# Optimization experiments

Measured on AMD Instinct MI355X. Metric: run time of the kernel, lower is better.

## Reference

```python
import math
import jax, jax.numpy as jnp
import numpy as np
from jax.scipy.special import gammaln, xlogy

HEADS = 8
DIM_KEY = 64
DIM_VALUE = 64
NUM_REL_POS_FEATURES = 192
DIM = 768
SEQ = 2048
BATCH = 2


def get_positional_embed(seq_len: int, feature_size: int) -> jnp.ndarray:
    # distances: [2n-1]
    distances = jnp.arange(-seq_len + 1, seq_len, dtype=jnp.float32)
    f = feature_size // 6  # 3 basis classes, then doubled with sign term
    absd = jnp.abs(distances)[:, None]  # [2n-1, 1]
    # exponential basis
    max_range = math.log(seq_len) / math.log(2.0)
    half_life = 2.0 ** jnp.linspace(3.0, max_range, f)[None, :]
    exp_feat = jnp.exp(-math.log(2.0) / half_life * absd)
    # central mask basis
    center_widths = 2.0 ** jnp.arange(1, f + 1, dtype=jnp.float32) - 1.0
    cmask = (center_widths[None, :] > absd).astype(jnp.float32)
    # gamma pdf basis
    stddev = seq_len / (2.0 * f)
    start_mean = seq_len / f
    mean = jnp.linspace(start_mean, float(seq_len), f)[None, :]
    concentration = (mean / stddev) ** 2
    rate = mean / stddev ** 2
    log_unnorm = xlogy(concentration - 1.0, absd) - rate * absd
    log_norm = gammaln(concentration) - concentration * jnp.log(rate)
    probs = jnp.exp(log_unnorm - log_norm) + 1e-8
    gamma_feat = probs / jnp.max(probs, axis=-1, keepdims=True)
    emb = jnp.concatenate([exp_feat, cmask, gamma_feat], axis=-1)  # [2n-1, 3f]
    return jnp.concatenate([emb, jnp.sign(distances)[:, None] * emb], axis=-1)  # [2n-1, 6f]


def relative_shift(x: jnp.ndarray) -> jnp.ndarray:
    # x: [b, h, n, 2n-1] -> [b, h, n, n] via Transformer-XL shift trick
    x = jnp.concatenate([jnp.zeros_like(x[..., :1]), x], axis=-1)
    b, h, t1, t2 = x.shape  # t2 = 2n
    x = x.reshape(b, h, t2, t1)[:, :, 1:, :].reshape(b, h, t1, t2 - 1)
    return x[..., : (t2 + 1) // 2]


def setup_inputs() -> dict:
    key = jax.random.key(0)
    ks = jax.random.split(key, 9)
    d_inner = HEADS * DIM_KEY
    d_vinner = HEADS * DIM_VALUE
    sc = 1.0 / math.sqrt(DIM)
    return {
        "x": jax.random.normal(ks[0], (BATCH, SEQ, DIM), dtype=jnp.float32),
        "Wq": jax.random.normal(ks[1], (DIM, d_inner), dtype=jnp.float32) * sc,
        "Wk": jax.random.normal(ks[2], (DIM, d_inner), dtype=jnp.float32) * sc,
        "Wv": jax.random.normal(ks[3], (DIM, d_vinner), dtype=jnp.float32) * sc,
        "Wrel": jax.random.normal(ks[4], (NUM_REL_POS_FEATURES, d_inner), dtype=jnp.float32) * (1.0 / math.sqrt(NUM_REL_POS_FEATURES)),
        "rel_content_bias": jax.random.normal(ks[5], (1, HEADS, 1, DIM_KEY), dtype=jnp.float32),
        "rel_pos_bias": jax.random.normal(ks[6], (1, HEADS, 1, DIM_KEY), dtype=jnp.float32),
        "Wo": jax.random.normal(ks[7], (d_vinner, DIM), dtype=jnp.float32) * (1.0 / math.sqrt(d_vinner)),
        "bo": jax.random.normal(ks[8], (DIM,), dtype=jnp.float32) * 0.01,
    }


def reference(x, Wq, Wk, Wv, Wrel, rel_content_bias, rel_pos_bias, Wo, bo):
    b, n, _ = x.shape
    scale = DIM_KEY ** -0.5
    # projections -> [b, h, n, d]
    q = (x @ Wq).reshape(b, n, HEADS, DIM_KEY).transpose(0, 2, 1, 3) * scale
    k = (x @ Wk).reshape(b, n, HEADS, DIM_KEY).transpose(0, 2, 1, 3)
    v = (x @ Wv).reshape(b, n, HEADS, DIM_VALUE).transpose(0, 2, 1, 3)
    content_logits = jnp.einsum("bhid,bhjd->bhij", q + rel_content_bias, k)
    positions = get_positional_embed(n, NUM_REL_POS_FEATURES)  # [2n-1, F]
    rel_k = (positions @ Wrel).reshape(2 * n - 1, HEADS, DIM_KEY).transpose(1, 0, 2)  # [h, 2n-1, d]
    rel_logits = jnp.einsum("bhid,hjd->bhij", q + rel_pos_bias, rel_k)
    rel_logits = relative_shift(rel_logits)  # [b, h, n, n]
    attn = jax.nn.softmax(content_logits + rel_logits, axis=-1)
    out = jnp.einsum("bhij,bhjd->bhid", attn, v)  # [b, h, n, dv]
    out = out.transpose(0, 2, 1, 3).reshape(b, n, HEADS * DIM_VALUE)
    return out @ Wo + bo
```

## Files before the change

kernel.cpp:

```cpp
#include <hip/hip_runtime.h>
#include <hip/hip_bf16.h>
#include <math.h>


typedef _Float16 f16x8 __attribute__((ext_vector_type(8)));
typedef _Float16 f16x4 __attribute__((ext_vector_type(4)));
typedef float f32x4 __attribute__((ext_vector_type(4)));

#define MFMA16(a, b, c) __builtin_amdgcn_mfma_f32_16x16x32_f16((a), (b), (c), 0, 0, 0)

#define GL16(gp, lp)                                                       \
  __builtin_amdgcn_global_load_lds(                                        \
      (const __attribute__((address_space(1))) void*)(gp),                 \
      (__attribute__((address_space(3))) void*)(lp), 16, 0, 0)

__device__ __forceinline__ float dpp_fmax16(float x) {
  int v;
  v = __builtin_amdgcn_update_dpp(0, __float_as_int(x), 0xB1, 0xf, 0xf, true);
  x = fmaxf(x, __int_as_float(v));
  v = __builtin_amdgcn_update_dpp(0, __float_as_int(x), 0x4E, 0xf, 0xf, true);
  x = fmaxf(x, __int_as_float(v));
  v = __builtin_amdgcn_update_dpp(0, __float_as_int(x), 0x141, 0xf, 0xf, true);
  x = fmaxf(x, __int_as_float(v));
  v = __builtin_amdgcn_update_dpp(0, __float_as_int(x), 0x140, 0xf, 0xf, true);
  x = fmaxf(x, __int_as_float(v));
  return x;
}

__global__ __launch_bounds__(256) void prep_kernel(
    const float* __restrict__ x, const float* __restrict__ Wq,
    const float* __restrict__ Wk, const float* __restrict__ Wv,
    const float* __restrict__ Wrel, const float* __restrict__ Wo,
    _Float16* __restrict__ xb, _Float16* __restrict__ wqkvt,
    _Float16* __restrict__ wrelt, _Float16* __restrict__ wot,
    _Float16* __restrict__ posb) {
  __shared__ float tile[32][33];
  const int t = threadIdx.x;
  int bid = blockIdx.x;
  if (bid < 3072) {
    const int idx = bid * 256 + t;
    float4 v = ((const float4*)x)[idx];
    f16x4 o;
    o[0] = (_Float16)v.x; o[1] = (_Float16)v.y; o[2] = (_Float16)v.z; o[3] = (_Float16)v.w;
    ((f16x4*)xb)[idx] = o;
    return;
  }
  bid -= 3072;
  if (bid < 1632) {
    const float* in; _Float16* out; int K_, N_, bx, by;
    if (bid < 1152) {
      const int z = bid / 384, rem = bid % 384;
      in = (z == 0) ? Wq : (z == 1) ? Wk : Wv;
      out = wqkvt + (size_t)z * 512 * 768;
      K_ = 768; N_ = 512; bx = rem & 15; by = rem >> 4;
    } else if (bid < 1248) {
      const int rem = bid - 1152;
      in = Wrel; out = wrelt;
      K_ = 192; N_ = 512; bx = rem & 15; by = rem >> 4;
    } else {
      const int rem = bid - 1248;
      in = Wo; out = wot;
      K_ = 512; N_ = 768; bx = rem % 24; by = rem / 24;
    }
    const int k0 = by * 32, n0 = bx * 32;
    const int tr = t >> 3, tc = (t & 7) * 4;
    float4 v = *(const float4*)(in + (size_t)(k0 + tr) * N_ + n0 + tc);
    tile[tr][tc] = v.x; tile[tr][tc + 1] = v.y; tile[tr][tc + 2] = v.z; tile[tr][tc + 3] = v.w;
    __syncthreads();
    f16x4 o;
    o[0] = (_Float16)tile[tc][tr];
    o[1] = (_Float16)tile[tc + 1][tr];
    o[2] = (_Float16)tile[tc + 2][tr];
    o[3] = (_Float16)tile[tc + 3][tr];
    *(f16x4*)(out + (size_t)(n0 + tr) * K_ + k0 + tc) = o;
    return;
  }
  bid -= 1632;
  const int lr = t >> 5, i = t & 31;
  const int r = bid * 8 + lr;
  _Float16* row = posb + (size_t)r * 192;
  if (r >= 4095) {
    row[i] = (_Float16)0.f; row[32 + i] = (_Float16)0.f; row[64 + i] = (_Float16)0.f;
    row[96 + i] = (_Float16)0.f; row[128 + i] = (_Float16)0.f; row[160 + i] = (_Float16)0.f;
    return;
  }
  const float dist = (float)(r - 2047);
  const float absd = fabsf(dist);
  const float sgn = (dist > 0.f) ? 1.f : ((dist < 0.f) ? -1.f : 0.f);
  const float e = 3.f + (float)i * (8.f / 31.f);
  const float expv = exp2f(-absd * exp2f(-e));
  const float cw = exp2f((float)(i + 1)) - 1.f;
  const float cm = (cw > absd) ? 1.f : 0.f;
  const float mean = 64.f * (float)(i + 1);
  const float conc = (mean / 32.f) * (mean / 32.f);
  const float rate = mean / 1024.f;
  const float lnrm = lgammaf(conc) - conc * logf(rate);
  const float lu = (conc - 1.f) * logf(absd) - rate * absd;
  float gv = expf(lu - lnrm) + 1e-8f;
  float mx = gv;
  mx = fmaxf(mx, __shfl_xor(mx, 1));
  mx = fmaxf(mx, __shfl_xor(mx, 2));
  mx = fmaxf(mx, __shfl_xor(mx, 4));
  mx = fmaxf(mx, __shfl_xor(mx, 8));
  mx = fmaxf(mx, __shfl_xor(mx, 16));
  gv /= mx;
  row[i] = (_Float16)expv;              row[32 + i] = (_Float16)cm;
  row[64 + i] = (_Float16)gv;           row[96 + i] = (_Float16)(sgn * expv);
  row[128 + i] = (_Float16)(sgn * cm);  row[160 + i] = (_Float16)(sgn * gv);
}

__global__ __launch_bounds__(256, 4) void gemm_qkvrel(
    const _Float16* __restrict__ xb, const _Float16* __restrict__ wqkvt,
    const _Float16* __restrict__ posb, const _Float16* __restrict__ wrelt,
    _Float16* __restrict__ qc, _Float16* __restrict__ qp,
    _Float16* __restrict__ kbo, _Float16* __restrict__ vt,
    _Float16* __restrict__ relk,
    const float* __restrict__ bc, const float* __restrict__ bp) {
  __shared__ __align__(16) _Float16 As[2][64 * 32];
  __shared__ __align__(16) _Float16 Bs[2][128 * 32];
  const int tid = threadIdx.x;
  const int w = tid >> 6, lane = tid & 63, g = lane >> 4, m = lane & 15;
  const int wr = w >> 1, wc = w & 1;
  const int bid = blockIdx.x;
  const bool isrel = bid >= 768;
  const _Float16* A; const _Float16* Bt; int K, row0, c0;
  if (isrel) {
    const int tt = bid - 768;
    A = posb; Bt = wrelt; K = 192;
    c0 = (tt & 3) * 128; row0 = (tt >> 2) * 64;
  } else {
    A = xb; Bt = wqkvt; K = 768;
    c0 = (bid % 12) * 128; row0 = (bid / 12) * 64;
  }

  const int arow = tid >> 2, asl = tid & 3;
  const int axor = asl ^ ((arow >> 1) & 3);
  const char* Ag = (const char*)(A + (size_t)(row0 + arow) * K) + (axor << 4);
  const int adst = (arow << 6) + (asl << 4);
  const int brow = w * 32 + (lane >> 2);
  const int bxor = asl ^ ((brow >> 1) & 3);
  const char* Bg = (const char*)(Bt + (size_t)(c0 + brow) * K) + (bxor << 4);
  const size_t bstep = (size_t)16 * K * 2;
  const int bdst = (brow << 6) + (asl << 4);

  int aoff[2], boff[4];
#pragma unroll
  for (int i = 0; i < 2; ++i) {
    const int ar = wr * 32 + i * 16 + m;
    aoff[i] = (ar << 6) + ((g ^ ((ar >> 1) & 3)) << 4);
  }
#pragma unroll
  for (int i = 0; i < 4; ++i) {
    const int br = wc * 64 + i * 16 + m;
    boff[i] = (br << 6) + ((g ^ ((br >> 1) & 3)) << 4);
  }

#define STAGEG(buf, k0v)                                       \
  GL16(Ag + ((k0v) << 1), (char*)As[buf] + adst);              \
  GL16(Bg + ((k0v) << 1), (char*)Bs[buf] + bdst);              \
  GL16(Bg + bstep + ((k0v) << 1), (char*)Bs[buf] + bdst + 1024);

  f32x4 acc[2][4] = {};
  STAGEG(0, 0);
  __syncthreads();
  const int nk = K >> 5;
  for (int ks = 0; ks < nk; ++ks) {
    const int cur = ks & 1;
    if (ks + 1 < nk) { STAGEG(cur ^ 1, (ks + 1) << 5); }
    const char* ap = (const char*)As[cur];
    const char* bp_ = (const char*)Bs[cur];
    f16x8 af[2], bf[4];
#pragma unroll
    for (int i = 0; i < 2; ++i) af[i] = *(const f16x8*)(ap + aoff[i]);
#pragma unroll
    for (int i = 0; i < 4; ++i) bf[i] = *(const f16x8*)(bp_ + boff[i]);
#pragma unroll
    for (int mi = 0; mi < 2; ++mi)
#pragma unroll
      for (int ni = 0; ni < 4; ++ni)
        acc[mi][ni] = MFMA16(af[mi], bf[ni], acc[mi][ni]);
    __syncthreads();
  }
#undef STAGEG

  if (isrel) {
#pragma unroll
    for (int ni = 0; ni < 4; ++ni) {
      const int col = c0 + wc * 64 + ni * 16 + m;
      const int hh = col >> 6, dk = col & 63;
#pragma unroll
      for (int mi = 0; mi < 2; ++mi)
#pragma unroll
        for (int r = 0; r < 4; ++r) {
          const int row = row0 + wr * 32 + mi * 16 + g * 4 + r;
          relk[((size_t)hh * 4096 + row) * 64 + dk] = (_Float16)acc[mi][ni][r];
        }
    }
  } else {
    const int proj = c0 >> 9;
#pragma unroll
    for (int ni = 0; ni < 4; ++ni) {
      const int col = c0 + wc * 64 + ni * 16 + m;
      const int c = col & 511, hh = c >> 6, dk = c & 63;
      float b0f = 0.f, b1f = 0.f;
      if (proj == 0) { b0f = bc[c]; b1f = bp[c]; }
      if (proj == 2) {
#pragma unroll
        for (int mi = 0; mi < 2; ++mi) {
          const int rowb = row0 + wr * 32 + mi * 16 + g * 4;
          const int bb = rowb >> 11, n = rowb & 2047;
          f16x4 pk;
#pragma unroll
          for (int r = 0; r < 4; ++r) pk[r] = (_Float16)acc[mi][ni][r];
          *(f16x4*)(vt + ((size_t)(bb * 8 + hh) * 64 + dk) * 2048 + n) = pk;
        }
      } else {
#pragma unroll
        for (int mi = 0; mi < 2; ++mi)
#pragma unroll
          for (int r = 0; r < 4; ++r) {
            const int row = row0 + wr * 32 + mi * 16 + g * 4 + r;
            const int bb = row >> 11, n = row & 2047;
            const size_t ad = ((size_t)(bb * 8 + hh) * 2048 + n) * 64 + dk;
            const float v = acc[mi][ni][r];
            if (proj == 0) {
              const float vs = v * 0.125f;
              qc[ad] = (_Float16)(vs + b0f);
              qp[ad] = (_Float16)(vs + b1f);
            } else {
              kbo[ad] = (_Float16)v;
            }
          }
      }
    }
  }
}

__global__ __launch_bounds__(256, 4) void gemm_out(
    const _Float16* __restrict__ A, const _Float16* __restrict__ Bt,
    const float* __restrict__ bias, float* __restrict__ outf) {
  __shared__ __align__(16) _Float16 As[2][64 * 32];
  __shared__ __align__(16) _Float16 Bs[2][128 * 32];
  const int tid = threadIdx.x;
  const int w = tid >> 6, lane = tid & 63, g = lane >> 4, m = lane & 15;
  const int wr = w >> 1, wc = w & 1;
  const int K = 512;
  const int row0 = blockIdx.y * 64;
  const int c0 = blockIdx.x * 128;

  const int arow = tid >> 2, asl = tid & 3;
  const int axor = asl ^ ((arow >> 1) & 3);
  const char* Ag = (const char*)(A + (size_t)(row0 + arow) * K) + (axor << 4);
  const int adst = (arow << 6) + (asl << 4);
  const int brow = w * 32 + (lane >> 2);
  const int bxor = asl ^ ((brow >> 1) & 3);
  const char* Bg = (const char*)(Bt + (size_t)(c0 + brow) * K) + (bxor << 4);
  const size_t bstep = (size_t)16 * K * 2;
  const int bdst = (brow << 6) + (asl << 4);

  int aoff[2], boff[4];
#pragma unroll
  for (int i = 0; i < 2; ++i) {
    const int ar = wr * 32 + i * 16 + m;
    aoff[i] = (ar << 6) + ((g ^ ((ar >> 1) & 3)) << 4);
  }
#pragma unroll
  for (int i = 0; i < 4; ++i) {
    const int br = wc * 64 + i * 16 + m;
    boff[i] = (br << 6) + ((g ^ ((br >> 1) & 3)) << 4);
  }

#define STAGEG(buf, k0v)                                       \
  GL16(Ag + ((k0v) << 1), (char*)As[buf] + adst);              \
  GL16(Bg + ((k0v) << 1), (char*)Bs[buf] + bdst);              \
  GL16(Bg + bstep + ((k0v) << 1), (char*)Bs[buf] + bdst + 1024);

  f32x4 acc[2][4] = {};
  STAGEG(0, 0);
  __syncthreads();
  const int nk = K >> 5;
  for (int ks = 0; ks < nk; ++ks) {
    const int cur = ks & 1;
    if (ks + 1 < nk) { STAGEG(cur ^ 1, (ks + 1) << 5); }
    const char* ap = (const char*)As[cur];
    const char* bp_ = (const char*)Bs[cur];
    f16x8 af[2], bf[4];
#pragma unroll
    for (int i = 0; i < 2; ++i) af[i] = *(const f16x8*)(ap + aoff[i]);
#pragma unroll
    for (int i = 0; i < 4; ++i) bf[i] = *(const f16x8*)(bp_ + boff[i]);
#pragma unroll
    for (int mi = 0; mi < 2; ++mi)
#pragma unroll
      for (int ni = 0; ni < 4; ++ni)
        acc[mi][ni] = MFMA16(af[mi], bf[ni], acc[mi][ni]);
    __syncthreads();
  }
#undef STAGEG

#pragma unroll
  for (int ni = 0; ni < 4; ++ni) {
    const int col = c0 + wc * 64 + ni * 16 + m;
    const float bv = bias[col];
#pragma unroll
    for (int mi = 0; mi < 2; ++mi)
#pragma unroll
      for (int r = 0; r < 4; ++r) {
        const int row = row0 + wr * 32 + mi * 16 + g * 4 + r;
        outf[(size_t)row * 768 + col] = acc[mi][ni][r] + bv;
      }
  }
}

__global__ __launch_bounds__(256, 3) void attn_kernel(
    const _Float16* __restrict__ qc, const _Float16* __restrict__ qp,
    const _Float16* __restrict__ kb, const _Float16* __restrict__ vtb,
    const _Float16* __restrict__ relkb, _Float16* __restrict__ attnb) {
  __shared__ __align__(16) char lds[50176];
  const int tid = threadIdx.x;
  const int w = tid >> 6, lane = tid & 63, g = lane >> 4, m = lane & 15;
  const int L = blockIdx.x;
  const int h = L & 7;
  const int r2 = L >> 3;
  const int b = r2 >> 5, xt = r2 & 31;
  const int bh = b * 8 + h;
  const int i0b = xt << 6;
  const int i0 = i0b + w * 16;
  const int dR = 1984 - i0b;

  const int srow = tid >> 3, ssl = tid & 7;
  const int sxr16 = (ssl ^ (srow & 7)) << 4;
  const int dst16 = (srow << 7) + (ssl << 4);
  const char* kgs = (const char*)kb + ((size_t)bh << 18) + sxr16;
  const char* rgs = (const char*)relkb + ((size_t)h << 19) + sxr16;

  char* Kb0 = lds;
  char* Kb1 = lds + 8192;
  char* Ring = lds + 16384;

#define STAGE_K(dstp, j0v)                                              \
  GL16(kgs + ((size_t)((j0v) + srow) << 7), (dstp) + dst16);            \
  GL16(kgs + ((size_t)((j0v) + srow + 32) << 7), (dstp) + dst16 + 4096);
#define STAGE_R(dstp, c)                                                       \
  GL16(rgs + ((size_t)(dR + ((c) << 6) + srow) << 7), (dstp) + dst16);         \
  GL16(rgs + ((size_t)(dR + ((c) << 6) + srow + 32) << 7), (dstp) + dst16 + 4096);

  STAGE_K(Kb0, 0);
  STAGE_R(Ring, 0);
  STAGE_R(Ring + 8192, 1);

  const size_t qbase = ((size_t)bh * 2048 + i0 + m) * 64 + g * 8;
  f16x8 qcf0 = *(const f16x8*)(qc + qbase);
  f16x8 qcf1 = *(const f16x8*)(qc + qbase + 32);
  f16x8 qpf0 = *(const f16x8*)(qp + qbase);
  f16x8 qpf1 = *(const f16x8*)(qp + qbase + 32);

  f16x8 onesv;
#pragma unroll
  for (int i = 0; i < 8; ++i) onesv[i] = (_Float16)1.f;

  __syncthreads();

  f32x4 acc_o[4] = {};
  f32x4 acc_l = {};
  float m_run[4];
#pragma unroll
  for (int r = 0; r < 4; ++r) m_run[r] = -1e30f;

  const int sx = m & 7;
  const int fo0 = (g ^ sx) << 4;
  const int fo1 = ((4 | g) ^ sx) << 4;
  const int lb0 = 48 - (w << 4);
  _Float16* Pl = (_Float16*)(lds + 40960 + w * 2304);

  char* rsA = Ring;
  char* rsB = Ring + 8192;
  char* rsC = Ring + 16384;

  for (int jt = 0; jt < 32; ++jt) {
    if (jt < 31) {
      char* kn = (jt & 1) ? Kb0 : Kb1;
      STAGE_K(kn, (jt + 1) << 6);
      STAGE_R(rsC, jt + 2);
    }
    const char* curK = (jt & 1) ? Kb1 : Kb0;
    __builtin_amdgcn_s_setprio(1);
    f32x4 sc[4] = {};
#pragma unroll
    for (int cf = 0; cf < 4; ++cf) {
      const char* kp = curK + ((m + (cf << 4)) << 7);
      sc[cf] = MFMA16(qcf0, *(const f16x8*)(kp + fo0), sc[cf]);
      sc[cf] = MFMA16(qcf1, *(const f16x8*)(kp + fo1), sc[cf]);
    }
    f32x4 rc[5] = {};
#pragma unroll
    for (int cf = 0; cf < 5; ++cf) {
      const int lb = lb0 + (cf << 4);
      const char* sp = (lb & 64) ? rsB : rsA;
      const char* rp = sp + (((lb & 63) + m) << 7);
      rc[cf] = MFMA16(qpf0, *(const f16x8*)(rp + fo0), rc[cf]);
      rc[cf] = MFMA16(qpf1, *(const f16x8*)(rp + fo1), rc[cf]);
    }
    __builtin_amdgcn_s_setprio(0);
#pragma unroll
    for (int r = 0; r < 4; ++r) {
      const int lr = g * 4 + r;
      const int u = 15 + m - lr;
      const int src = (g << 4) | (u & 15);
      const bool hi = (m > lr);
      float sh0 = __shfl(rc[0][r], src);
      float sh1 = __shfl(rc[1][r], src);
      float sh2 = __shfl(rc[2][r], src);
      float sh3 = __shfl(rc[3][r], src);
      float sh4 = __shfl(rc[4][r], src);
      sc[0][r] += hi ? sh1 : sh0;
      sc[1][r] += hi ? sh2 : sh1;
      sc[2][r] += hi ? sh3 : sh2;
      sc[3][r] += hi ? sh4 : sh3;
    }
    float mx[4];
#pragma unroll
    for (int r = 0; r < 4; ++r) {
      float v = fmaxf(fmaxf(sc[0][r], sc[1][r]), fmaxf(sc[2][r], sc[3][r]));
      mx[r] = dpp_fmax16(v);
    }
    const bool need = (mx[0] > m_run[0] + 8.f) || (mx[1] > m_run[1] + 8.f) ||
                      (mx[2] > m_run[2] + 8.f) || (mx[3] > m_run[3] + 8.f);
    if (__any(need)) {
#pragma unroll
      for (int r = 0; r < 4; ++r) {
        const float mnew = fmaxf(m_run[r], mx[r]);
        const float corr = __expf(m_run[r] - mnew);
        m_run[r] = mnew;
#pragma unroll
        for (int cf = 0; cf < 4; ++cf) acc_o[cf][r] *= corr;
        acc_l[r] *= corr;
      }
    }
    float P[4][4];
#pragma unroll
    for (int r = 0; r < 4; ++r)
#pragma unroll
      for (int cf = 0; cf < 4; ++cf)
        P[cf][r] = __expf(sc[cf][r] - m_run[r]);
#pragma unroll
    for (int cf = 0; cf < 4; ++cf)
#pragma unroll
      for (int r = 0; r < 4; ++r)
        Pl[(g * 4 + r) * 72 + cf * 16 + m] = (_Float16)P[cf][r];
    const size_t vbase = ((size_t)bh * 64 + m) * 2048 + ((size_t)jt << 6) + g * 8;
    __builtin_amdgcn_s_setprio(1);
#pragma unroll
    for (int ks = 0; ks < 2; ++ks) {
      f16x8 pa = *(const f16x8*)((const char*)Pl + m * 144 + ks * 64 + (g << 4));
#pragma unroll
      for (int cf = 0; cf < 4; ++cf) {
        f16x8 vf = *(const f16x8*)(vtb + vbase + (size_t)cf * 32768 + ks * 32);
        acc_o[cf] = MFMA16(pa, vf, acc_o[cf]);
      }
      acc_l = MFMA16(pa, onesv, acc_l);
    }
    __builtin_amdgcn_s_setprio(0);
    __syncthreads();
    char* tmp = rsA; rsA = rsB; rsB = rsC; rsC = tmp;
  }
#pragma unroll
  for (int cf = 0; cf < 4; ++cf)
#pragma unroll
    for (int r = 0; r < 4; ++r) {
      const int i = i0 + g * 4 + r;
      const float o = acc_o[cf][r] / acc_l[r];
      attnb[((size_t)(b * 2048 + i)) * 512 + h * 64 + cf * 16 + m] = (_Float16)o;
    }
#undef STAGE_K
#undef STAGE_R
}

extern "C" void kernel_launch(void* const* d_in, const int* in_sizes, int n_in,
                              void* d_out, int out_size, void* d_ws, size_t ws_size,
                              hipStream_t stream) {
  (void)in_sizes; (void)n_in; (void)out_size; (void)ws_size;
  const float* x    = (const float*)d_in[0];
  const float* Wq   = (const float*)d_in[1];
  const float* Wk   = (const float*)d_in[2];
  const float* Wv   = (const float*)d_in[3];
  const float* Wrel = (const float*)d_in[4];
  const float* bc   = (const float*)d_in[5];
  const float* bp   = (const float*)d_in[6];
  const float* Wo   = (const float*)d_in[7];
  const float* bo   = (const float*)d_in[8];
  float* out = (float*)d_out;

  char* ws = (char*)d_ws;
  size_t off = 0;
  auto alloc = [&](size_t bytes) -> void* {
    void* p = ws + off;
    off += (bytes + 255) & ~(size_t)255;
    return p;
  };
  _Float16* xb     = (_Float16*)alloc(4096ull * 768 * 2);
  _Float16* wqkvt  = (_Float16*)alloc(1536ull * 768 * 2);
  _Float16* wrelt  = (_Float16*)alloc(512ull * 192 * 2);
  _Float16* wot    = (_Float16*)alloc(768ull * 512 * 2);
  _Float16* posb   = (_Float16*)alloc(4096ull * 192 * 2);
  _Float16* qcb    = (_Float16*)alloc(16ull * 2048 * 64 * 2);
  _Float16* qpb    = (_Float16*)alloc(16ull * 2048 * 64 * 2);
  _Float16* kbb    = (_Float16*)alloc(16ull * 2048 * 64 * 2);
  _Float16* vtb    = (_Float16*)alloc(16ull * 64 * 2048 * 2);
  _Float16* relkb  = (_Float16*)alloc(8ull * 4096 * 64 * 2);
  _Float16* attnb  = (_Float16*)alloc(4096ull * 512 * 2);

  prep_kernel<<<5216, 256, 0, stream>>>(x, Wq, Wk, Wv, Wrel, Wo,
                                        xb, wqkvt, wrelt, wot, posb);

  gemm_qkvrel<<<1024, 256, 0, stream>>>(xb, wqkvt, posb, wrelt,
                                        qcb, qpb, kbb, vtb, relkb, bc, bp);

  attn_kernel<<<512, 256, 0, stream>>>(qcb, qpb, kbb, vtb, relkb, attnb);

  gemm_out<<<dim3(6, 64), 256, 0, stream>>>(attnb, wot, bo, out);
}
```

Before: 220.4 us.

## Stage V tiles through LDS and pack rel-logit shuffles into fp16 pairs

The V tile is now double-buffered in LDS using async global-to-LDS loads, the same way as K. This replaces the direct per-lane global loads of V inside the PV MFMA loop. The relative-position logits are packed into fp16 pairs before the cross-lane shuffle, cutting shuffle count from 5 to 3 per row at the cost of rounding the rel logits to fp16. LDS grows from about 50 KB to 65 KB and launch bounds drop from 3 to 2 blocks per CU, which reduces occupancy.

```diff
diff --git a/kernel.cpp b/kernel.cpp
--- a/kernel.cpp
+++ b/kernel.cpp
@@ -5,6 +5,7 @@
 
 typedef _Float16 f16x8 __attribute__((ext_vector_type(8)));
 typedef _Float16 f16x4 __attribute__((ext_vector_type(4)));
+typedef __fp16 fp16x2 __attribute__((ext_vector_type(2)));
 typedef float f32x4 __attribute__((ext_vector_type(4)));
 
 #define MFMA16(a, b, c) __builtin_amdgcn_mfma_f32_16x16x32_f16((a), (b), (c), 0, 0, 0)
@@ -312,11 +313,11 @@
   }
 }
 
-__global__ __launch_bounds__(256, 3) void attn_kernel(
+__global__ __launch_bounds__(256, 2) void attn_kernel(
     const _Float16* __restrict__ qc, const _Float16* __restrict__ qp,
     const _Float16* __restrict__ kb, const _Float16* __restrict__ vtb,
     const _Float16* __restrict__ relkb, _Float16* __restrict__ attnb) {
-  __shared__ __align__(16) char lds[50176];
+  __shared__ __align__(16) char lds[66560];
   const int tid = threadIdx.x;
   const int w = tid >> 6, lane = tid & 63, g = lane >> 4, m = lane & 15;
   const int L = blockIdx.x;
@@ -332,20 +333,27 @@
   const int sxr16 = (ssl ^ (srow & 7)) << 4;
   const int dst16 = (srow << 7) + (ssl << 4);
   const char* kgs = (const char*)kb + ((size_t)bh << 18) + sxr16;
+  const char* vgs = (const char*)vtb + ((size_t)bh << 18) + ((size_t)srow << 12) + sxr16;
   const char* rgs = (const char*)relkb + ((size_t)h << 19) + sxr16;
 
   char* Kb0 = lds;
   char* Kb1 = lds + 8192;
-  char* Ring = lds + 16384;
+  char* Vb0 = lds + 16384;
+  char* Vb1 = lds + 24576;
+  char* Ring = lds + 32768;
 
 #define STAGE_K(dstp, j0v)                                              \
   GL16(kgs + ((size_t)((j0v) + srow) << 7), (dstp) + dst16);            \
   GL16(kgs + ((size_t)((j0v) + srow + 32) << 7), (dstp) + dst16 + 4096);
+#define STAGE_V(dstp, j0v)                                              \
+  GL16(vgs + ((j0v) << 1), (dstp) + dst16);                             \
+  GL16(vgs + ((size_t)32 << 12) + ((j0v) << 1), (dstp) + dst16 + 4096);
 #define STAGE_R(dstp, c)                                                       \
   GL16(rgs + ((size_t)(dR + ((c) << 6) + srow) << 7), (dstp) + dst16);         \
   GL16(rgs + ((size_t)(dR + ((c) << 6) + srow + 32) << 7), (dstp) + dst16 + 4096);
 
   STAGE_K(Kb0, 0);
+  STAGE_V(Vb0, 0);
   STAGE_R(Ring, 0);
   STAGE_R(Ring + 8192, 1);
 
@@ -371,7 +379,7 @@
   const int fo0 = (g ^ sx) << 4;
   const int fo1 = ((4 | g) ^ sx) << 4;
   const int lb0 = 48 - (w << 4);
-  _Float16* Pl = (_Float16*)(lds + 40960 + w * 2304);
+  _Float16* Pl = (_Float16*)(lds + 57344 + w * 2304);
 
   char* rsA = Ring;
   char* rsB = Ring + 8192;
@@ -380,10 +388,14 @@
   for (int jt = 0; jt < 32; ++jt) {
     if (jt < 31) {
       char* kn = (jt & 1) ? Kb0 : Kb1;
-      STAGE_K(kn, (jt + 1) << 6);
+      char* vn = (jt & 1) ? Vb0 : Vb1;
+      const int j0n = (jt + 1) << 6;
+      STAGE_K(kn, j0n);
+      STAGE_V(vn, j0n);
       STAGE_R(rsC, jt + 2);
     }
     const char* curK = (jt & 1) ? Kb1 : Kb0;
+    const char* curV = (jt & 1) ? Vb1 : Vb0;
     __builtin_amdgcn_s_setprio(1);
     f32x4 sc[4] = {};
 #pragma unroll
@@ -408,15 +420,17 @@
       const int u = 15 + m - lr;
       const int src = (g << 4) | (u & 15);
       const bool hi = (m > lr);
-      float sh0 = __shfl(rc[0][r], src);
-      float sh1 = __shfl(rc[1][r], src);
-      float sh2 = __shfl(rc[2][r], src);
-      float sh3 = __shfl(rc[3][r], src);
-      float sh4 = __shfl(rc[4][r], src);
-      sc[0][r] += hi ? sh1 : sh0;
-      sc[1][r] += hi ? sh2 : sh1;
-      sc[2][r] += hi ? sh3 : sh2;
-      sc[3][r] += hi ? sh4 : sh3;
+      union { fp16x2 v; int i; __fp16 h[2]; } p01, p23, p4;
+      p01.v = __builtin_amdgcn_cvt_pkrtz(rc[0][r], rc[1][r]);
+      p23.v = __builtin_amdgcn_cvt_pkrtz(rc[2][r], rc[3][r]);
+      p4.v  = __builtin_amdgcn_cvt_pkrtz(rc[4][r], rc[4][r]);
+      p01.i = __shfl(p01.i, src);
+      p23.i = __shfl(p23.i, src);
+      p4.i  = __shfl(p4.i, src);
+      sc[0][r] += (float)(hi ? p01.h[1] : p01.h[0]);
+      sc[1][r] += (float)(hi ? p23.h[0] : p01.h[1]);
+      sc[2][r] += (float)(hi ? p23.h[1] : p23.h[0]);
+      sc[3][r] += (float)(hi ? p4.h[0] : p23.h[1]);
     }
     float mx[4];
 #pragma unroll
@@ -448,15 +462,14 @@
 #pragma unroll
       for (int r = 0; r < 4; ++r)
         Pl[(g * 4 + r) * 72 + cf * 16 + m] = (_Float16)P[cf][r];
-    const size_t vbase = ((size_t)bh * 64 + m) * 2048 + ((size_t)jt << 6) + g * 8;
     __builtin_amdgcn_s_setprio(1);
 #pragma unroll
     for (int ks = 0; ks < 2; ++ks) {
       f16x8 pa = *(const f16x8*)((const char*)Pl + m * 144 + ks * 64 + (g << 4));
 #pragma unroll
       for (int cf = 0; cf < 4; ++cf) {
-        f16x8 vf = *(const f16x8*)(vtb + vbase + (size_t)cf * 32768 + ks * 32);
-        acc_o[cf] = MFMA16(pa, vf, acc_o[cf]);
+        const char* vp = curV + ((m + (cf << 4)) << 7);
+        acc_o[cf] = MFMA16(pa, *(const f16x8*)(vp + (ks ? fo1 : fo0)), acc_o[cf]);
       }
       acc_l = MFMA16(pa, onesv, acc_l);
     }
@@ -473,6 +486,7 @@
       attnb[((size_t)(b * 2048 + i)) * 512 + h * 64 + cf * 16 + m] = (_Float16)o;
     }
 #undef STAGE_K
+#undef STAGE_V
 #undef STAGE_R
 }
 
```

After: 188.8 us. 14.3% less time.
